# Kernel tuning notes

Hardware: AMD Instinct MI355X
Metric: run time of the kernel (lower is better)

The kernel has to match this reference:

```python
import jax, jax.numpy as jnp
import numpy as np

B, N, A, M, H, KD, VD, O = 256, 2048, 256, 256, 8, 32, 32, 256
EPS = 1e-10

def setup_inputs() -> dict:
    key = jax.random.key(0)
    ks = jax.random.split(key, 8)
    return {
        "q_data": jax.random.normal(ks[0], (B, N, A), dtype=jnp.float32),
        "m_data": jax.random.normal(ks[1], (B, N, M), dtype=jnp.float32),
        "q_mask": jnp.ones((B, N, 1), dtype=jnp.float32),
        "bias": jnp.zeros((B, 1, N), dtype=jnp.float32),
        "query_w": 0.02 * jax.random.normal(ks[2], (A, H, KD), dtype=jnp.float32),
        "key_w": 0.02 * jax.random.normal(ks[3], (M, KD), dtype=jnp.float32),
        "value_w": 0.02 * jax.random.normal(ks[4], (M, VD), dtype=jnp.float32),
        "gating_w": 0.02 * jax.random.normal(ks[5], (A, H, VD), dtype=jnp.float32),
        "gating_b": jnp.zeros((H, VD), dtype=jnp.float32),
        "output_w": 0.02 * jax.random.normal(ks[6], (H, VD, O), dtype=jnp.float32),
        "output_b": jnp.zeros((O,), dtype=jnp.float32),
    }

def reference(q_data, m_data, q_mask, bias, query_w, key_w, value_w,
              gating_w, gating_b, output_w, output_b):
    # masked mean over the query axis: q_mask [B,N,1] broadcasts over channels
    q_avg = jnp.sum(q_mask * q_data, axis=1) / (jnp.sum(q_mask, axis=1) + EPS)  # [B,A]
    kd = query_w.shape[-1]
    q = jnp.einsum('ba,ahc->bhc', q_avg, query_w) * kd ** (-0.5)  # [B,H,KD]
    k = jnp.einsum('bka,ac->bkc', m_data, key_w)                  # [B,N,KD]
    v = jnp.einsum('bka,ac->bkc', m_data, value_w)                # [B,N,VD]
    # the incoming `bias` arg is overwritten by the module, as in the original
    attn_bias = 1e9 * (q_mask[:, None, :, 0] - 1.0)               # [B,1,N]
    logits = jnp.einsum('bhc,bkc->bhk', q, k) + attn_bias         # [B,H,N]
    weights = jax.nn.softmax(logits, axis=-1)
    weighted_avg = jnp.einsum('bhk,bkc->bhc', weights, v)         # [B,H,VD]
    # gating == True
    gate = jax.nn.sigmoid(jnp.einsum('bqc,chv->bqhv', q_data, gating_w) + gating_b)
    gated = weighted_avg[:, None] * gate                          # [B,N,H,VD]
    out = jnp.einsum('bqhc,hco->bqo', gated, output_w) + output_b # [B,N,O]
    return out
```

## Files before the change

### kernel.cpp

```cpp
#include <hip/hip_runtime.h>

#define B_ 256
#define N_ 2048
#define A_ 256
#define M_ 256
#define H_ 8
#define KD_ 32
#define VD_ 32
#define O_ 256

typedef float f32x4 __attribute__((ext_vector_type(4)));
typedef __bf16 bf16x8 __attribute__((ext_vector_type(8)));
typedef unsigned short u16x8 __attribute__((ext_vector_type(8)));

union FragU { u16x8 u; bf16x8 b; };

__device__ __forceinline__ unsigned short f2bf(float f) {
  union { __bf16 b; unsigned short u; } c;
  c.b = (__bf16)f;
  return c.u;
}
__device__ __forceinline__ float bf2f(unsigned short h) {
  return __uint_as_float(((unsigned int)h) << 16);
}

__device__ __forceinline__ void gll16(const void* gsrc, void* ldst) {
  __builtin_amdgcn_global_load_lds(
      (const __attribute__((address_space(1))) void*)gsrc,
      (__attribute__((address_space(3))) void*)ldst, 16, 0, 0);
}

__global__ void pack_weights(const float* __restrict__ gating_w,
                             const float* __restrict__ output_w,
                             const float* __restrict__ key_w,
                             const float* __restrict__ value_w,
                             unsigned short* __restrict__ wg,
                             unsigned short* __restrict__ wo,
                             unsigned short* __restrict__ wkv) {
  int idx = blockIdx.x * 256 + threadIdx.x;
  int j = idx & 7;
  int lane = (idx >> 3) & 63;
  int rest = idx >> 9;
  int kc = rest & 7, ct = rest >> 3;
  int row = kc * 32 + ((lane >> 4) << 3) + j;
  int col = ct * 16 + (lane & 15);
  wg[idx] = f2bf(gating_w[row * 256 + col]);
  wo[idx] = f2bf(output_w[row * 256 + col]);
  if (idx < 16384) {
    float v = (col < 32) ? key_w[row * 32 + col] : value_w[row * 32 + (col - 32)];
    wkv[idx] = f2bf(v);
  }
}

__global__ void reduce_q(const float* __restrict__ qd, const float* __restrict__ qm,
                         const float* __restrict__ qw, float* __restrict__ q_out) {
  int b = blockIdx.x;
  int t = threadIdx.x;
  int l = t & 63, g = t >> 6;
  const float* qdb = qd + (size_t)b * N_ * A_;
  const float* qmb = qm + (size_t)b * N_;
  f32x4 sum = {0.f, 0.f, 0.f, 0.f};
  float msum = 0.f;
  for (int n = g; n < N_; n += 16) {
    float m = qmb[n];
    msum += m;
    f32x4 v = *(const f32x4*)(qdb + (size_t)n * A_ + l * 4);
    sum += m * v;
  }
  __shared__ float s[16][256];
  __shared__ float ms[16];
  __shared__ float qavg[256];
  *(f32x4*)&s[g][l * 4] = sum;
  if (l == 0) ms[g] = msum;
  __syncthreads();
  if (t < 256) {
    float tot = 0.f;
#pragma unroll
    for (int k = 0; k < 16; k++) tot += s[k][t];
    float mt = 0.f;
#pragma unroll
    for (int k = 0; k < 16; k++) mt += ms[k];
    qavg[t] = tot / (mt + 1e-10f);
  }
  __syncthreads();
  if (t < 256) {
    float acc = 0.f;
    for (int a2 = 0; a2 < 256; a2++) acc += qavg[a2] * qw[a2 * 256 + t];
    q_out[b * 256 + t] = acc * 0.17677669529663687f;
  }
}

__global__ void kv_gemm(const float* __restrict__ md,
                        const unsigned short* __restrict__ wkv,
                        unsigned short* __restrict__ k_ws,
                        unsigned short* __restrict__ v_ws) {
  int t = threadIdx.x;
  int w = t >> 6, l = t & 63, q = l >> 4, l15 = l & 15;
  size_t r0 = (size_t)blockIdx.x * 128;
  int b = (int)(r0 >> 11);
  int n0 = (int)(r0 & 2047);
  f32x4 acc[2][4] = {};
  for (int kc = 0; kc < 8; kc++) {
    FragU bfr[4];
#pragma unroll
    for (int ct = 0; ct < 4; ct++)
      bfr[ct].u = *(const u16x8*)(wkv + (((ct * 8 + kc) * 64 + l) << 3));
    FragU af[2];
#pragma unroll
    for (int rt = 0; rt < 2; rt++) {
      size_t row = r0 + (size_t)(w * 32 + rt * 16 + l15);
      const float4* s4 = (const float4*)(md + row * 256 + kc * 32 + q * 8);
      float4 u0 = s4[0], u1 = s4[1];
      af[rt].u = (u16x8){f2bf(u0.x), f2bf(u0.y), f2bf(u0.z), f2bf(u0.w),
                         f2bf(u1.x), f2bf(u1.y), f2bf(u1.z), f2bf(u1.w)};
    }
#pragma unroll
    for (int ct = 0; ct < 4; ct++) {
      acc[0][ct] = __builtin_amdgcn_mfma_f32_16x16x32_bf16(af[0].b, bfr[ct].b, acc[0][ct], 0, 0, 0);
      acc[1][ct] = __builtin_amdgcn_mfma_f32_16x16x32_bf16(af[1].b, bfr[ct].b, acc[1][ct], 0, 0, 0);
    }
  }
#pragma unroll
  for (int rt = 0; rt < 2; rt++)
#pragma unroll
    for (int ct = 0; ct < 4; ct++)
#pragma unroll
      for (int r = 0; r < 4; r++) {
        int rloc = w * 32 + rt * 16 + q * 4 + r;
        if (ct < 2) {
          k_ws[(r0 + rloc) * 32 + ct * 16 + l15] = f2bf(acc[rt][ct][r]);
        } else {
          v_ws[((size_t)b * 32 + (ct - 2) * 16 + l15) * N_ + (n0 + rloc)] = f2bf(acc[rt][ct][r]);
        }
      }
}

__global__ void attn_softmax(const unsigned short* __restrict__ k_ws,
                             const unsigned short* __restrict__ v_ws,
                             const float* __restrict__ qv,
                             const float* __restrict__ qm,
                             float* __restrict__ wa) {
  int b = blockIdx.x, t = threadIdx.x;
  __shared__ float lg[8][2048];
  __shared__ float red[4][256];
  __shared__ float inv_s[8];
  const float* qb = qv + b * 256;
  const float* qmb = qm + (size_t)b * N_;
  for (int n = t; n < N_; n += 1024) {
    const u16x8* kr = (const u16x8*)(k_ws + ((size_t)(b * N_ + n)) * 32);
    u16x8 ka = kr[0], kb2 = kr[1], kc2 = kr[2], kd2 = kr[3];
    float kf[32];
#pragma unroll
    for (int j = 0; j < 8; j++) {
      kf[j]      = bf2f(ka[j]);
      kf[8 + j]  = bf2f(kb2[j]);
      kf[16 + j] = bf2f(kc2[j]);
      kf[24 + j] = bf2f(kd2[j]);
    }
    float bias_n = 1e9f * (qmb[n] - 1.0f);
#pragma unroll
    for (int h = 0; h < 8; h++) {
      float d = 0.f;
#pragma unroll
      for (int c = 0; c < 32; c++) d += qb[h * 32 + c] * kf[c];
      lg[h][n] = d + bias_n;
    }
  }
  __syncthreads();
  if (t < 256) {
    int h = t >> 5, i = t & 31;
    float m = -3.0e38f;
    for (int n = i; n < N_; n += 32) m = fmaxf(m, lg[h][n]);
#pragma unroll
    for (int off = 16; off; off >>= 1) m = fmaxf(m, __shfl_xor(m, off));
    float s = 0.f;
    for (int n = i; n < N_; n += 32) {
      float e = __expf(lg[h][n] - m);
      lg[h][n] = e;
      s += e;
    }
#pragma unroll
    for (int off = 16; off; off >>= 1) s += __shfl_xor(s, off);
    if (i == 0) inv_s[h] = 1.0f / s;
  }
  __syncthreads();
  {
    int c = t & 31, h = (t >> 5) & 7, nq = t >> 8;
    const u16x8* vb = (const u16x8*)(v_ws + ((size_t)b * 32 + c) * N_ + nq * 512);
    const f32x4* lg4 = (const f32x4*)&lg[h][nq * 512];
    float acc = 0.f;
#pragma unroll 4
    for (int n8 = 0; n8 < 64; n8++) {
      u16x8 vv = vb[n8];
      f32x4 p0 = lg4[n8 * 2], p1 = lg4[n8 * 2 + 1];
      acc += p0[0] * bf2f(vv[0]);
      acc += p0[1] * bf2f(vv[1]);
      acc += p0[2] * bf2f(vv[2]);
      acc += p0[3] * bf2f(vv[3]);
      acc += p1[0] * bf2f(vv[4]);
      acc += p1[1] * bf2f(vv[5]);
      acc += p1[2] * bf2f(vv[6]);
      acc += p1[3] * bf2f(vv[7]);
    }
    red[nq][t & 255] = acc;
  }
  __syncthreads();
  if (t < 256) {
    float r = red[0][t] + red[1][t] + red[2][t] + red[3][t];
    wa[b * 256 + t] = r * inv_s[t >> 5];
  }
}

__launch_bounds__(256, 2)
__global__ void gate_out(const float* __restrict__ qd,
                         const unsigned short* __restrict__ wg,
                         const unsigned short* __restrict__ wo,
                         const float* __restrict__ wa,
                         const float* __restrict__ gb,
                         const float* __restrict__ ob,
                         float* __restrict__ out) {
  int blk = blockIdx.x;
  int b = blk >> 4, tile = blk & 15;
  int t = threadIdx.x;
  int w = t >> 6, l = t & 63, q = l >> 4, l15 = l & 15;
  __shared__ __attribute__((aligned(16))) unsigned short wsg[8192];
  __shared__ __attribute__((aligned(16))) unsigned short wso[8192];
  __shared__ __attribute__((aligned(16))) unsigned short Pt[4][2][16][40];
  __shared__ float wa_s[256], gb_s[256], ob_s[256];
  wa_s[t] = wa[b * 256 + t];
  gb_s[t] = gb[t];
  ob_s[t] = ob[t];
  size_t rowbase = (size_t)b * N_ + tile * 128;

  {
    const char* wgb = (const char*)wg;
    const char* wob = (const char*)wo;
#pragma unroll
    for (int i = 0; i < 4; i++) {
      int ch = i * 4 + w;
      gll16(wgb + ch * 1024 + l * 16, (char*)wsg + ch * 1024);
      gll16(wob + ch * 8192 + l * 16, (char*)wso + ch * 1024);
    }
  }

  FragU af[2][8];
#pragma unroll
  for (int rt = 0; rt < 2; rt++) {
    const float* src = qd + (rowbase + (size_t)(w * 32 + rt * 16 + l15)) * 256 + q * 8;
#pragma unroll
    for (int kc = 0; kc < 8; kc++) {
      float4 u0 = *(const float4*)(src + kc * 32);
      float4 u1 = *(const float4*)(src + kc * 32 + 4);
      af[rt][kc].u = (u16x8){f2bf(u0.x), f2bf(u0.y), f2bf(u0.z), f2bf(u0.w),
                             f2bf(u1.x), f2bf(u1.y), f2bf(u1.z), f2bf(u1.w)};
    }
  }
  f32x4 acc[2][16] = {};
  __syncthreads();

  for (int g = 0; g < 8; g++) {
    f32x4 gacc[2][2] = {};
#pragma unroll
    for (int kc = 0; kc < 8; kc++) {
      FragU b0, b1;
      b0.u = *(const u16x8*)(wsg + (kc * 64 + l) * 8);
      b1.u = *(const u16x8*)(wsg + ((8 + kc) * 64 + l) * 8);
      gacc[0][0] = __builtin_amdgcn_mfma_f32_16x16x32_bf16(af[0][kc].b, b0.b, gacc[0][0], 0, 0, 0);
      gacc[0][1] = __builtin_amdgcn_mfma_f32_16x16x32_bf16(af[0][kc].b, b1.b, gacc[0][1], 0, 0, 0);
      gacc[1][0] = __builtin_amdgcn_mfma_f32_16x16x32_bf16(af[1][kc].b, b0.b, gacc[1][0], 0, 0, 0);
      gacc[1][1] = __builtin_amdgcn_mfma_f32_16x16x32_bf16(af[1][kc].b, b1.b, gacc[1][1], 0, 0, 0);
    }
#pragma unroll
    for (int rt = 0; rt < 2; rt++)
#pragma unroll
      for (int ctl = 0; ctl < 2; ctl++) {
        int colg = ctl * 16 + l15;
        int col = g * 32 + colg;
        float wav = wa_s[col], gbv = gb_s[col];
#pragma unroll
        for (int r = 0; r < 4; r++) {
          float x = gacc[rt][ctl][r] + gbv;
          float gate = 1.0f / (1.0f + __expf(-x));
          Pt[w][rt][q * 4 + r][colg] = f2bf(wav * gate);
        }
      }
    FragU pf[2];
#pragma unroll
    for (int rt = 0; rt < 2; rt++)
      pf[rt].u = *(const u16x8*)&Pt[w][rt][l15][q * 8];

    __syncthreads();
    if (g < 7) {
      const char* wgb = (const char*)wg + (size_t)(g + 1) * 16384;
#pragma unroll
      for (int i = 0; i < 4; i++) {
        int ch = i * 4 + w;
        gll16(wgb + ch * 1024 + l * 16, (char*)wsg + ch * 1024);
      }
    }
#pragma unroll
    for (int ct = 0; ct < 16; ct++) {
      FragU bo;
      bo.u = *(const u16x8*)(wso + (ct * 64 + l) * 8);
      acc[0][ct] = __builtin_amdgcn_mfma_f32_16x16x32_bf16(pf[0].b, bo.b, acc[0][ct], 0, 0, 0);
      acc[1][ct] = __builtin_amdgcn_mfma_f32_16x16x32_bf16(pf[1].b, bo.b, acc[1][ct], 0, 0, 0);
    }
    __syncthreads();
    if (g < 7) {
      const char* wob = (const char*)wo + (size_t)(g + 1) * 1024;
#pragma unroll
      for (int i = 0; i < 4; i++) {
        int ch = i * 4 + w;
        gll16(wob + ch * 8192 + l * 16, (char*)wso + ch * 1024);
      }
    }
  }
#pragma unroll
  for (int rt = 0; rt < 2; rt++)
#pragma unroll
    for (int ct = 0; ct < 16; ct++) {
      int col = ct * 16 + l15;
      float obv = ob_s[col];
      size_t orow = (rowbase + (size_t)(w * 32 + rt * 16 + q * 4)) * 256 + col;
#pragma unroll
      for (int r = 0; r < 4; r++)
        out[orow + (size_t)r * 256] = acc[rt][ct][r] + obv;
    }
}

extern "C" void kernel_launch(void* const* d_in, const int* in_sizes, int n_in,
                              void* d_out, int out_size, void* d_ws, size_t ws_size,
                              hipStream_t stream) {
  const float* q_data   = (const float*)d_in[0];
  const float* m_data   = (const float*)d_in[1];
  const float* q_mask   = (const float*)d_in[2];
  const float* query_w  = (const float*)d_in[4];
  const float* key_w    = (const float*)d_in[5];
  const float* value_w  = (const float*)d_in[6];
  const float* gating_w = (const float*)d_in[7];
  const float* gating_b = (const float*)d_in[8];
  const float* output_w = (const float*)d_in[9];
  const float* output_b = (const float*)d_in[10];
  float* out = (float*)d_out;

  char* ws = (char*)d_ws;
  float* q_ws            = (float*)(ws);
  float* wa_ws           = (float*)(ws + (256 << 10));
  unsigned short* wg_ws  = (unsigned short*)(ws + (512 << 10));
  unsigned short* wo_ws  = (unsigned short*)(ws + (640 << 10));
  unsigned short* wkv_ws = (unsigned short*)(ws + (768 << 10));
  unsigned short* k_wsp  = (unsigned short*)(ws + (800 << 10));
  unsigned short* v_wsp  = (unsigned short*)(ws + (800 << 10) + ((size_t)32 << 20));

  pack_weights<<<256, 256, 0, stream>>>(gating_w, output_w, key_w, value_w,
                                        wg_ws, wo_ws, wkv_ws);
  reduce_q<<<B_, 1024, 0, stream>>>(q_data, q_mask, query_w, q_ws);
  kv_gemm<<<(B_ * N_) / 128, 256, 0, stream>>>(m_data, wkv_ws, k_wsp, v_wsp);
  attn_softmax<<<B_, 1024, 0, stream>>>(k_wsp, v_wsp, q_ws, q_mask, wa_ws);
  gate_out<<<(B_ * N_) / 128, 256, 0, stream>>>(q_data, wg_ws, wo_ws, wa_ws,
                                                gating_b, output_b, out);
}
```

Baseline: 1.458 ms.

## Double-buffer gate_out weights, vectorize V stores, merge prep kernels

```diff
diff --git a/kernel.cpp b/kernel.cpp
--- a/kernel.cpp
+++ b/kernel.cpp
@@ -12,6 +12,7 @@
 typedef float f32x4 __attribute__((ext_vector_type(4)));
 typedef __bf16 bf16x8 __attribute__((ext_vector_type(8)));
 typedef unsigned short u16x8 __attribute__((ext_vector_type(8)));
+typedef unsigned short u16x4 __attribute__((ext_vector_type(4)));
 
 union FragU { u16x8 u; bf16x8 b; };
 
@@ -30,30 +31,31 @@
       (__attribute__((address_space(3))) void*)ldst, 16, 0, 0);
 }
 
-__global__ void pack_weights(const float* __restrict__ gating_w,
-                             const float* __restrict__ output_w,
-                             const float* __restrict__ key_w,
-                             const float* __restrict__ value_w,
-                             unsigned short* __restrict__ wg,
-                             unsigned short* __restrict__ wo,
-                             unsigned short* __restrict__ wkv) {
-  int idx = blockIdx.x * 256 + threadIdx.x;
-  int j = idx & 7;
-  int lane = (idx >> 3) & 63;
-  int rest = idx >> 9;
-  int kc = rest & 7, ct = rest >> 3;
-  int row = kc * 32 + ((lane >> 4) << 3) + j;
-  int col = ct * 16 + (lane & 15);
-  wg[idx] = f2bf(gating_w[row * 256 + col]);
-  wo[idx] = f2bf(output_w[row * 256 + col]);
-  if (idx < 16384) {
-    float v = (col < 32) ? key_w[row * 32 + col] : value_w[row * 32 + (col - 32)];
-    wkv[idx] = f2bf(v);
-  }
-}
-
-__global__ void reduce_q(const float* __restrict__ qd, const float* __restrict__ qm,
-                         const float* __restrict__ qw, float* __restrict__ q_out) {
+__global__ void prep(const float* __restrict__ qd, const float* __restrict__ qm,
+                     const float* __restrict__ qw, float* __restrict__ q_out,
+                     const float* __restrict__ gating_w,
+                     const float* __restrict__ output_w,
+                     const float* __restrict__ key_w,
+                     const float* __restrict__ value_w,
+                     unsigned short* __restrict__ wg,
+                     unsigned short* __restrict__ wo,
+                     unsigned short* __restrict__ wkv) {
+  if (blockIdx.x >= 256) {
+    int idx = (blockIdx.x - 256) * 1024 + threadIdx.x;
+    int j = idx & 7;
+    int lane = (idx >> 3) & 63;
+    int rest = idx >> 9;
+    int kc = rest & 7, ct = rest >> 3;
+    int row = kc * 32 + ((lane >> 4) << 3) + j;
+    int col = ct * 16 + (lane & 15);
+    wg[idx] = f2bf(gating_w[row * 256 + col]);
+    wo[idx] = f2bf(output_w[row * 256 + col]);
+    if (idx < 16384) {
+      float v = (col < 32) ? key_w[row * 32 + col] : value_w[row * 32 + (col - 32)];
+      wkv[idx] = f2bf(v);
+    }
+    return;
+  }
   int b = blockIdx.x;
   int t = threadIdx.x;
   int l = t & 63, g = t >> 6;
@@ -121,18 +123,22 @@
     }
   }
 #pragma unroll
-  for (int rt = 0; rt < 2; rt++)
-#pragma unroll
-    for (int ct = 0; ct < 4; ct++)
+  for (int rt = 0; rt < 2; rt++) {
+#pragma unroll
+    for (int ct = 0; ct < 2; ct++)
 #pragma unroll
       for (int r = 0; r < 4; r++) {
         int rloc = w * 32 + rt * 16 + q * 4 + r;
-        if (ct < 2) {
-          k_ws[(r0 + rloc) * 32 + ct * 16 + l15] = f2bf(acc[rt][ct][r]);
-        } else {
-          v_ws[((size_t)b * 32 + (ct - 2) * 16 + l15) * N_ + (n0 + rloc)] = f2bf(acc[rt][ct][r]);
-        }
+        k_ws[(r0 + rloc) * 32 + ct * 16 + l15] = f2bf(acc[rt][ct][r]);
       }
+#pragma unroll
+    for (int ct = 2; ct < 4; ct++) {
+      int nbase = n0 + w * 32 + rt * 16 + q * 4;
+      u16x4 pv = {f2bf(acc[rt][ct][0]), f2bf(acc[rt][ct][1]),
+                  f2bf(acc[rt][ct][2]), f2bf(acc[rt][ct][3])};
+      *(u16x4*)&v_ws[((size_t)b * 32 + (ct - 2) * 16 + l15) * N_ + nbase] = pv;
+    }
+  }
 }
 
 __global__ void attn_softmax(const unsigned short* __restrict__ k_ws,
@@ -223,8 +229,8 @@
   int b = blk >> 4, tile = blk & 15;
   int t = threadIdx.x;
   int w = t >> 6, l = t & 63, q = l >> 4, l15 = l & 15;
-  __shared__ __attribute__((aligned(16))) unsigned short wsg[8192];
-  __shared__ __attribute__((aligned(16))) unsigned short wso[8192];
+  __shared__ __attribute__((aligned(16))) unsigned short wsg[2][8192];
+  __shared__ __attribute__((aligned(16))) unsigned short wso[2][8192];
   __shared__ __attribute__((aligned(16))) unsigned short Pt[4][2][16][40];
   __shared__ float wa_s[256], gb_s[256], ob_s[256];
   wa_s[t] = wa[b * 256 + t];
@@ -238,8 +244,8 @@
 #pragma unroll
     for (int i = 0; i < 4; i++) {
       int ch = i * 4 + w;
-      gll16(wgb + ch * 1024 + l * 16, (char*)wsg + ch * 1024);
-      gll16(wob + ch * 8192 + l * 16, (char*)wso + ch * 1024);
+      gll16(wgb + ch * 1024 + l * 16, (char*)&wsg[0][0] + ch * 1024);
+      gll16(wob + ch * 8192 + l * 16, (char*)&wso[0][0] + ch * 1024);
     }
   }
 
@@ -259,12 +265,23 @@
   __syncthreads();
 
   for (int g = 0; g < 8; g++) {
+    int cur = g & 1;
+    if (g < 7) {
+      const char* wgb = (const char*)wg + (size_t)(g + 1) * 16384;
+      const char* wob = (const char*)wo + (size_t)(g + 1) * 1024;
+#pragma unroll
+      for (int i = 0; i < 4; i++) {
+        int ch = i * 4 + w;
+        gll16(wgb + ch * 1024 + l * 16, (char*)&wsg[cur ^ 1][0] + ch * 1024);
+        gll16(wob + ch * 8192 + l * 16, (char*)&wso[cur ^ 1][0] + ch * 1024);
+      }
+    }
     f32x4 gacc[2][2] = {};
 #pragma unroll
     for (int kc = 0; kc < 8; kc++) {
       FragU b0, b1;
-      b0.u = *(const u16x8*)(wsg + (kc * 64 + l) * 8);
-      b1.u = *(const u16x8*)(wsg + ((8 + kc) * 64 + l) * 8);
+      b0.u = *(const u16x8*)(&wsg[cur][0] + (kc * 64 + l) * 8);
+      b1.u = *(const u16x8*)(&wsg[cur][0] + ((8 + kc) * 64 + l) * 8);
       gacc[0][0] = __builtin_amdgcn_mfma_f32_16x16x32_bf16(af[0][kc].b, b0.b, gacc[0][0], 0, 0, 0);
       gacc[0][1] = __builtin_amdgcn_mfma_f32_16x16x32_bf16(af[0][kc].b, b1.b, gacc[0][1], 0, 0, 0);
       gacc[1][0] = __builtin_amdgcn_mfma_f32_16x16x32_bf16(af[1][kc].b, b0.b, gacc[1][0], 0, 0, 0);
@@ -288,32 +305,14 @@
 #pragma unroll
     for (int rt = 0; rt < 2; rt++)
       pf[rt].u = *(const u16x8*)&Pt[w][rt][l15][q * 8];
-
-    __syncthreads();
-    if (g < 7) {
-      const char* wgb = (const char*)wg + (size_t)(g + 1) * 16384;
-#pragma unroll
-      for (int i = 0; i < 4; i++) {
-        int ch = i * 4 + w;
-        gll16(wgb + ch * 1024 + l * 16, (char*)wsg + ch * 1024);
-      }
-    }
 #pragma unroll
     for (int ct = 0; ct < 16; ct++) {
       FragU bo;
-      bo.u = *(const u16x8*)(wso + (ct * 64 + l) * 8);
+      bo.u = *(const u16x8*)(&wso[cur][0] + (ct * 64 + l) * 8);
       acc[0][ct] = __builtin_amdgcn_mfma_f32_16x16x32_bf16(pf[0].b, bo.b, acc[0][ct], 0, 0, 0);
       acc[1][ct] = __builtin_amdgcn_mfma_f32_16x16x32_bf16(pf[1].b, bo.b, acc[1][ct], 0, 0, 0);
     }
     __syncthreads();
-    if (g < 7) {
-      const char* wob = (const char*)wo + (size_t)(g + 1) * 1024;
-#pragma unroll
-      for (int i = 0; i < 4; i++) {
-        int ch = i * 4 + w;
-        gll16(wob + ch * 8192 + l * 16, (char*)wso + ch * 1024);
-      }
-    }
   }
 #pragma unroll
   for (int rt = 0; rt < 2; rt++)
@@ -352,9 +351,9 @@
   unsigned short* k_wsp  = (unsigned short*)(ws + (800 << 10));
   unsigned short* v_wsp  = (unsigned short*)(ws + (800 << 10) + ((size_t)32 << 20));
 
-  pack_weights<<<256, 256, 0, stream>>>(gating_w, output_w, key_w, value_w,
-                                        wg_ws, wo_ws, wkv_ws);
-  reduce_q<<<B_, 1024, 0, stream>>>(q_data, q_mask, query_w, q_ws);
+  prep<<<320, 1024, 0, stream>>>(q_data, q_mask, query_w, q_ws,
+                                 gating_w, output_w, key_w, value_w,
+                                 wg_ws, wo_ws, wkv_ws);
   kv_gemm<<<(B_ * N_) / 128, 256, 0, stream>>>(m_data, wkv_ws, k_wsp, v_wsp);
   attn_softmax<<<B_, 1024, 0, stream>>>(k_wsp, v_wsp, q_ws, q_mask, wa_ws);
   gate_out<<<(B_ * N_) / 128, 256, 0, stream>>>(q_data, wg_ws, wo_ws, wa_ws,
```

Measured after the change: 1.480 ms. Within noise of the previous version (+1.5%).
